# Kernel optimization log

Measured on AMD Instinct MI355X. Metric: run time of the kernel, lower is better.

Reference implementation:

```python
import jax, jax.numpy as jnp
import numpy as np

N = 100000
E = 1600000
IN_FEAT, HID, OUT = 256, 64, 32


def setup_inputs() -> dict:
    key = jax.random.key(0)
    k = jax.random.split(key, 6)
    x = jax.random.normal(k[0], (N, IN_FEAT), dtype=jnp.float32)
    edge_index = jax.random.randint(k[1], (2, E), 0, N, dtype=jnp.int64)
    # fc1: Linear(in_feat, hidden_feat)
    fc1_w = jax.random.normal(k[2], (HID, IN_FEAT), dtype=jnp.float32) / np.sqrt(IN_FEAT)
    fc1_b = jnp.zeros((HID,), dtype=jnp.float32)
    # GCNConv(hidden_feat, out_feat): weight [hid, out], bias [out]
    gcn_w = jax.random.normal(k[3], (HID, OUT), dtype=jnp.float32) / np.sqrt(HID)
    gcn_b = jnp.zeros((OUT,), dtype=jnp.float32)
    return {"x": x, "edge_index": edge_index, "fc1_w": fc1_w, "fc1_b": fc1_b,
            "gcn_w": gcn_w, "gcn_b": gcn_b}


def reference(x, edge_index, fc1_w, fc1_b, gcn_w, gcn_b):
    n = x.shape[0]
    # fc1: dense linear
    h = x @ fc1_w.T + fc1_b                      # [N, HID]
    # GCNConv linear transform
    hw = h @ gcn_w                               # [N, OUT]
    # add self-loops (PyG default add_self_loops=True)
    loop = jnp.arange(n, dtype=edge_index.dtype)
    src = jnp.concatenate([edge_index[0], loop])  # [E+N]
    dst = jnp.concatenate([edge_index[1], loop])
    # symmetric degree normalization: deg computed on dst (in-degree incl. self-loops)
    deg = jax.ops.segment_sum(jnp.ones_like(dst, dtype=hw.dtype), dst, num_segments=n)
    dinv = jnp.where(deg > 0, jax.lax.rsqrt(deg), 0.0)
    norm = dinv[src] * dinv[dst]                  # [E+N]
    # gather source features, scale, scatter-add to destinations
    msgs = hw[src] * norm[:, None]                # [E+N, OUT]
    out = jax.ops.segment_sum(msgs, dst, num_segments=n) + gcn_b
    return out
```

## Files before the change

kernel.cpp:

```cpp
#include <hip/hip_runtime.h>
#include <hip/hip_fp16.h>

constexpr int IN_FEAT = 256;
constexpr int HID     = 64;
constexpr int OUT     = 32;

typedef _Float16 half8 __attribute__((ext_vector_type(8)));
typedef float    f32x4 __attribute__((ext_vector_type(4)));

__global__ __launch_bounds__(256) void prep_W(
    const float* __restrict__ fc1_w,
    const float* __restrict__ fc1_b,
    const float* __restrict__ gcn_w,
    _Float16* __restrict__ wsw,
    float* __restrict__ bhw)
{
    int idx = blockIdx.x * 256 + threadIdx.x;
    int k = idx >> 5;
    int c = idx & 31;
    float acc = 0.f;
#pragma unroll
    for (int h = 0; h < HID; ++h)
        acc += fc1_w[h * IN_FEAT + k] * gcn_w[h * OUT + c];
    wsw[c * 256 + (((k >> 3) ^ (c & 7)) << 3) + (k & 7)] = (_Float16)acc;

    if (idx < OUT) {
        float b = 0.f;
#pragma unroll
        for (int h = 0; h < HID; ++h)
            b += fc1_b[h] * gcn_w[h * OUT + idx];
        bhw[idx] = b;
    }
}

__global__ __launch_bounds__(256) void zero_cnt(int* __restrict__ cnt, int n)
{
    int i = blockIdx.x * 256 + threadIdx.x;
    if (i < n) cnt[i] = 0;
}

__global__ __launch_bounds__(256) void count_deg(
    const int* __restrict__ dst, int* __restrict__ cnt, int E)
{
    int e = blockIdx.x * 256 + threadIdx.x;
    if (e < E) atomicAdd(&cnt[dst[e]], 1);
}

__global__ __launch_bounds__(256) void make_dinv(
    const int* __restrict__ cnt, float* __restrict__ dinv, int n)
{
    int i = blockIdx.x * 256 + threadIdx.x;
    if (i < n) dinv[i] = rsqrtf((float)(cnt[i] + 1));
}

__global__ __launch_bounds__(256) void gemm_mfma(
    const float* __restrict__ x,
    const _Float16* __restrict__ wsw,
    const float* __restrict__ bhw,
    const float* __restrict__ dinv,
    const float* __restrict__ gcn_b,
    _Float16* __restrict__ hw2,
    _Float16* __restrict__ oacc,
    int n)
{
    __shared__ __align__(16) _Float16 xs[64 * 256];
    __shared__ __align__(16) _Float16 wt[32 * 256];

    int t = threadIdx.x;

    {
        const float4* wg = reinterpret_cast<const float4*>(wsw);
        float4* wl = reinterpret_cast<float4*>(wt);
#pragma unroll
        for (int i = 0; i < 4; ++i)
            wl[t + 256 * i] = wg[t + 256 * i];
    }

    int row0 = blockIdx.x * 64;
    {
        int hwid = t >> 5;
        int lk   = t & 31;
        const float4* xg = reinterpret_cast<const float4*>(x);
        float4 A[8], B[8];
#pragma unroll
        for (int g = 0; g < 8; ++g) {
            int r = g * 8 + hwid;
            int row = row0 + r;
            A[g] = make_float4(0.f, 0.f, 0.f, 0.f);
            B[g] = make_float4(0.f, 0.f, 0.f, 0.f);
            if (row < n) {
                const float4* p = xg + (size_t)row * 64 + lk * 2;
                A[g] = p[0];
                B[g] = p[1];
            }
        }
        char* xsb = reinterpret_cast<char*>(xs);
#pragma unroll
        for (int g = 0; g < 8; ++g) {
            int r = g * 8 + hwid;
            half8 h;
            h[0] = (_Float16)A[g].x; h[1] = (_Float16)A[g].y;
            h[2] = (_Float16)A[g].z; h[3] = (_Float16)A[g].w;
            h[4] = (_Float16)B[g].x; h[5] = (_Float16)B[g].y;
            h[6] = (_Float16)B[g].z; h[7] = (_Float16)B[g].w;
            int slot = lk ^ (r & 7);
            *reinterpret_cast<half8*>(xsb + r * 512 + slot * 16) = h;
        }
    }
    __syncthreads();

    int l = t & 63;
    int w = t >> 6;
    int lr   = l & 15;
    int acol = l >> 4;
    int arow = (w << 4) | lr;
    int axor = arow & 7;
    int bxor = lr & 7;

    const char* xsb = reinterpret_cast<const char*>(xs);
    const char* wtb = reinterpret_cast<const char*>(wt);

    f32x4 acc0 = {0.f, 0.f, 0.f, 0.f};
    f32x4 acc1 = {0.f, 0.f, 0.f, 0.f};
#pragma unroll
    for (int ks = 0; ks < 8; ++ks) {
        int ak = (ks << 2) | acol;
        half8 Af = *reinterpret_cast<const half8*>(xsb + arow * 512 + ((ak ^ axor) << 4));
        half8 B0 = *reinterpret_cast<const half8*>(wtb + lr * 512 + ((ak ^ bxor) << 4));
        half8 B1 = *reinterpret_cast<const half8*>(wtb + (lr + 16) * 512 + ((ak ^ bxor) << 4));
        acc0 = __builtin_amdgcn_mfma_f32_16x16x32_f16(Af, B0, acc0, 0, 0, 0);
        acc1 = __builtin_amdgcn_mfma_f32_16x16x32_f16(Af, B1, acc1, 0, 0, 0);
    }

    int c0 = lr;
    int orow0 = row0 + (w << 4) + (acol << 2);
    float b0  = bhw[c0];
    float b1  = bhw[c0 + 16];
    float gb0 = gcn_b[c0];
    float gb1 = gcn_b[c0 + 16];
#pragma unroll
    for (int i = 0; i < 4; ++i) {
        int row = orow0 + i;
        if (row < n) {
            float h0 = acc0[i] + b0;
            float h1 = acc1[i] + b1;
            hw2[(size_t)row * OUT + c0]      = (_Float16)h0;
            hw2[(size_t)row * OUT + 16 + c0] = (_Float16)h1;
            float di = dinv[row];
            float d2 = di * di;
            oacc[(size_t)row * OUT + c0]      = (_Float16)(gb0 + d2 * h0);
            oacc[(size_t)row * OUT + 16 + c0] = (_Float16)(gb1 + d2 * h1);
        }
    }
}

__global__ __launch_bounds__(256) void scatter_f16(
    const int* __restrict__ src, const int* __restrict__ dst,
    const float* __restrict__ dinv,
    const __half2* __restrict__ hw2,
    __half2* __restrict__ oacc,
    int E)
{
    int t = blockIdx.x * 256 + threadIdx.x;
    int e = t >> 4;
    int c = t & 15;
    if (e >= E) return;
    int s = src[e];
    int d = dst[e];
    float w = dinv[s] * dinv[d];
    __half2 hv = hw2[(size_t)s * 16 + c];
    __half2 val = __floats2half2_rn(w * __low2float(hv), w * __high2float(hv));
    unsafeAtomicAdd(&oacc[(size_t)d * 16 + c], val);
}

__global__ __launch_bounds__(256) void convert_out(
    const __half2* __restrict__ oacc, float2* __restrict__ out, int n16)
{
    int i = blockIdx.x * 256 + threadIdx.x;
    if (i >= n16) return;
    __half2 h = oacc[i];
    out[i] = make_float2(__low2float(h), __high2float(h));
}

extern "C" void kernel_launch(void* const* d_in, const int* in_sizes, int n_in,
                              void* d_out, int out_size, void* d_ws, size_t ws_size,
                              hipStream_t stream)
{
    const float* x      = (const float*)d_in[0];
    const int*   eidx   = (const int*)d_in[1];
    const float* fc1_w  = (const float*)d_in[2];
    const float* fc1_b  = (const float*)d_in[3];
    const float* gcn_w  = (const float*)d_in[4];
    const float* gcn_b  = (const float*)d_in[5];
    float* out = (float*)d_out;

    int n = in_sizes[0] / IN_FEAT;
    int E = in_sizes[1] / 2;
    const int* src = eidx;
    const int* dst = eidx + E;

    auto align4 = [](size_t v) { return (v + 3) & ~(size_t)3; };
    float* ws = (float*)d_ws;
    size_t o = 0;
    _Float16* wsw  = (_Float16*)(ws + o); o = align4(o + 4096);
    float*    bhw  = ws + o;              o = align4(o + OUT);
    float*    dinv = ws + o;              o = align4(o + n);
    int*      cnt  = (int*)(ws + o);      o = align4(o + n);
    _Float16* hw2  = (_Float16*)(ws + o); o = align4(o + (size_t)n * OUT / 2);
    _Float16* oacc = (_Float16*)(ws + o); o = align4(o + (size_t)n * OUT / 2);
    (void)ws_size;

    dim3 blk(256);
    prep_W<<<dim3((IN_FEAT * OUT) / 256), blk, 0, stream>>>(fc1_w, fc1_b, gcn_w, wsw, bhw);
    zero_cnt<<<dim3((n + 255) / 256), blk, 0, stream>>>(cnt, n);
    count_deg<<<dim3((E + 255) / 256), blk, 0, stream>>>(dst, cnt, E);
    make_dinv<<<dim3((n + 255) / 256), blk, 0, stream>>>(cnt, dinv, n);
    gemm_mfma<<<dim3((n + 63) / 64), blk, 0, stream>>>(
        x, wsw, bhw, dinv, gcn_b, hw2, oacc, n);
    long long sthreads = (long long)E * 16;
    scatter_f16<<<dim3((int)((sthreads + 255) / 256)), blk, 0, stream>>>(
        src, dst, dinv, (const __half2*)hw2, (__half2*)oacc, E);
    int n16 = n * OUT / 2;
    convert_out<<<dim3((n16 + 255) / 256), blk, 0, stream>>>(
        (const __half2*)oacc, (float2*)out, n16);
}
```

Baseline: 337.8 us.

## Bin edges by destination bucket and accumulate scatter in shared memory

Replaces per-node global degree atomics and the global fp16 atomic scatter with a coarse counting sort of edges into 128-node destination buckets. Per-bucket kernels then compute degrees and accumulate messages in fp32 shared-memory slices, writing the final output directly. This also removes the separate convert kernel. Separately, the GEMM reads the weight matrix straight from global/L2 instead of staging it in LDS. The costs are an extra binning pass with global atomics, extra edge storage, a single-block scan, and load imbalance when buckets hold different edge counts.

```diff
diff --git a/kernel.cpp b/kernel.cpp
--- a/kernel.cpp
+++ b/kernel.cpp
@@ -4,6 +4,8 @@
 constexpr int IN_FEAT = 256;
 constexpr int HID     = 64;
 constexpr int OUT     = 32;
+constexpr int BSH     = 7;
+constexpr int BR      = 1 << BSH;
 
 typedef _Float16 half8 __attribute__((ext_vector_type(8)));
 typedef float    f32x4 __attribute__((ext_vector_type(4)));
@@ -12,7 +14,7 @@
     const float* __restrict__ fc1_w,
     const float* __restrict__ fc1_b,
     const float* __restrict__ gcn_w,
-    _Float16* __restrict__ wsw,
+    _Float16* __restrict__ wlin,
     float* __restrict__ bhw)
 {
     int idx = blockIdx.x * 256 + threadIdx.x;
@@ -22,7 +24,7 @@
 #pragma unroll
     for (int h = 0; h < HID; ++h)
         acc += fc1_w[h * IN_FEAT + k] * gcn_w[h * OUT + c];
-    wsw[c * 256 + (((k >> 3) ^ (c & 7)) << 3) + (k & 7)] = (_Float16)acc;
+    wlin[c * 256 + k] = (_Float16)acc;
 
     if (idx < OUT) {
         float b = 0.f;
@@ -33,29 +35,85 @@
     }
 }
 
-__global__ __launch_bounds__(256) void zero_cnt(int* __restrict__ cnt, int n)
+__global__ __launch_bounds__(256) void zero_i32(int* __restrict__ p, int n)
 {
     int i = blockIdx.x * 256 + threadIdx.x;
-    if (i < n) cnt[i] = 0;
-}
-
-__global__ __launch_bounds__(256) void count_deg(
-    const int* __restrict__ dst, int* __restrict__ cnt, int E)
+    if (i < n) p[i] = 0;
+}
+
+__global__ __launch_bounds__(256) void bucket_count(
+    const int* __restrict__ dst, int* __restrict__ bcnt, int E)
 {
     int e = blockIdx.x * 256 + threadIdx.x;
-    if (e < E) atomicAdd(&cnt[dst[e]], 1);
-}
-
-__global__ __launch_bounds__(256) void make_dinv(
-    const int* __restrict__ cnt, float* __restrict__ dinv, int n)
-{
-    int i = blockIdx.x * 256 + threadIdx.x;
-    if (i < n) dinv[i] = rsqrtf((float)(cnt[i] + 1));
+    if (e < E) atomicAdd(&bcnt[dst[e] >> BSH], 1);
+}
+
+__global__ __launch_bounds__(256) void bucket_scan(
+    const int* __restrict__ bcnt, int* __restrict__ off, int* __restrict__ cur,
+    int NB)
+{
+    int t = threadIdx.x;
+    int i = t * 4;
+    int c0 = (i     < NB) ? bcnt[i]     : 0;
+    int c1 = (i + 1 < NB) ? bcnt[i + 1] : 0;
+    int c2 = (i + 2 < NB) ? bcnt[i + 2] : 0;
+    int c3 = (i + 3 < NB) ? bcnt[i + 3] : 0;
+    int s = c0 + c1 + c2 + c3;
+    int lane = t & 63;
+    int incl = s;
+    for (int d = 1; d < 64; d <<= 1) {
+        int u = __shfl_up(incl, d, 64);
+        if (lane >= d) incl += u;
+    }
+    __shared__ int wtot[4];
+    if (lane == 63) wtot[t >> 6] = incl;
+    __syncthreads();
+    int w = t >> 6;
+    int wbase = 0;
+    for (int j = 0; j < 4; ++j) if (j < w) wbase += wtot[j];
+    int e0 = wbase + incl - s;
+
+    if (i     < NB) { off[i]     = e0;                cur[i]     = e0; }
+    if (i + 1 < NB) { off[i + 1] = e0 + c0;           cur[i + 1] = e0 + c0; }
+    if (i + 2 < NB) { off[i + 2] = e0 + c0 + c1;      cur[i + 2] = e0 + c0 + c1; }
+    if (i + 3 < NB) { off[i + 3] = e0 + c0 + c1 + c2; cur[i + 3] = e0 + c0 + c1 + c2; }
+    if (t == 0) off[NB] = wtot[0] + wtot[1] + wtot[2] + wtot[3];
+}
+
+__global__ __launch_bounds__(256) void bin_edges(
+    const int* __restrict__ src, const int* __restrict__ dst,
+    int* __restrict__ cur, int2* __restrict__ edata, int E)
+{
+    int e = blockIdx.x * 256 + threadIdx.x;
+    if (e >= E) return;
+    int s = src[e];
+    int d = dst[e];
+    int pos = atomicAdd(&cur[d >> BSH], 1);
+    edata[pos] = make_int2(s, d);
+}
+
+__global__ __launch_bounds__(256) void deg_dinv(
+    const int2* __restrict__ edata, const int* __restrict__ off,
+    float* __restrict__ dinv, int n)
+{
+    __shared__ int lcnt[BR];
+    int b = blockIdx.x;
+    int t = threadIdx.x;
+    if (t < BR) lcnt[t] = 0;
+    __syncthreads();
+    int beg = off[b], end = off[b + 1];
+    for (int e = beg + t; e < end; e += 256)
+        atomicAdd(&lcnt[edata[e].y & (BR - 1)], 1);
+    __syncthreads();
+    if (t < BR) {
+        int node = (b << BSH) + t;
+        if (node < n) dinv[node] = rsqrtf((float)(lcnt[t] + 1));
+    }
 }
 
 __global__ __launch_bounds__(256) void gemm_mfma(
     const float* __restrict__ x,
-    const _Float16* __restrict__ wsw,
+    const _Float16* __restrict__ wlin,
     const float* __restrict__ bhw,
     const float* __restrict__ dinv,
     const float* __restrict__ gcn_b,
@@ -64,19 +122,10 @@
     int n)
 {
     __shared__ __align__(16) _Float16 xs[64 * 256];
-    __shared__ __align__(16) _Float16 wt[32 * 256];
-
-    int t = threadIdx.x;
-
-    {
-        const float4* wg = reinterpret_cast<const float4*>(wsw);
-        float4* wl = reinterpret_cast<float4*>(wt);
-#pragma unroll
-        for (int i = 0; i < 4; ++i)
-            wl[t + 256 * i] = wg[t + 256 * i];
-    }
-
+
+    int t = threadIdx.x;
     int row0 = blockIdx.x * 64;
+
     {
         int hwid = t >> 5;
         int lk   = t & 31;
@@ -115,10 +164,10 @@
     int acol = l >> 4;
     int arow = (w << 4) | lr;
     int axor = arow & 7;
-    int bxor = lr & 7;
 
     const char* xsb = reinterpret_cast<const char*>(xs);
-    const char* wtb = reinterpret_cast<const char*>(wt);
+    const _Float16* wb0 = wlin + lr * 256;
+    const _Float16* wb1 = wlin + (lr + 16) * 256;
 
     f32x4 acc0 = {0.f, 0.f, 0.f, 0.f};
     f32x4 acc1 = {0.f, 0.f, 0.f, 0.f};
@@ -126,8 +175,8 @@
     for (int ks = 0; ks < 8; ++ks) {
         int ak = (ks << 2) | acol;
         half8 Af = *reinterpret_cast<const half8*>(xsb + arow * 512 + ((ak ^ axor) << 4));
-        half8 B0 = *reinterpret_cast<const half8*>(wtb + lr * 512 + ((ak ^ bxor) << 4));
-        half8 B1 = *reinterpret_cast<const half8*>(wtb + (lr + 16) * 512 + ((ak ^ bxor) << 4));
+        half8 B0 = *reinterpret_cast<const half8*>(wb0 + (ak << 3));
+        half8 B1 = *reinterpret_cast<const half8*>(wb1 + (ak << 3));
         acc0 = __builtin_amdgcn_mfma_f32_16x16x32_f16(Af, B0, acc0, 0, 0, 0);
         acc1 = __builtin_amdgcn_mfma_f32_16x16x32_f16(Af, B1, acc1, 0, 0, 0);
     }
@@ -154,32 +203,50 @@
     }
 }
 
-__global__ __launch_bounds__(256) void scatter_f16(
-    const int* __restrict__ src, const int* __restrict__ dst,
-    const float* __restrict__ dinv,
-    const __half2* __restrict__ hw2,
-    __half2* __restrict__ oacc,
-    int E)
-{
-    int t = blockIdx.x * 256 + threadIdx.x;
-    int e = t >> 4;
-    int c = t & 15;
-    if (e >= E) return;
-    int s = src[e];
-    int d = dst[e];
-    float w = dinv[s] * dinv[d];
-    __half2 hv = hw2[(size_t)s * 16 + c];
-    __half2 val = __floats2half2_rn(w * __low2float(hv), w * __high2float(hv));
-    unsafeAtomicAdd(&oacc[(size_t)d * 16 + c], val);
-}
-
-__global__ __launch_bounds__(256) void convert_out(
-    const __half2* __restrict__ oacc, float2* __restrict__ out, int n16)
-{
-    int i = blockIdx.x * 256 + threadIdx.x;
-    if (i >= n16) return;
-    __half2 h = oacc[i];
-    out[i] = make_float2(__low2float(h), __high2float(h));
+__global__ __launch_bounds__(256) void scatter_bucket(
+    const int2* __restrict__ edata, const int* __restrict__ off,
+    const float* __restrict__ dinv, const _Float16* __restrict__ hw2,
+    const _Float16* __restrict__ oacc, float* __restrict__ out, int n)
+{
+    __shared__ float slice[BR * OUT];
+
+    int b = blockIdx.x;
+    int t = threadIdx.x;
+    for (int i = t; i < BR * OUT; i += 256) slice[i] = 0.f;
+    __syncthreads();
+
+    int beg = off[b], end = off[b + 1];
+    int g = t >> 5;
+    int c = t & 31;
+
+    auto process = [&](int e) {
+        int2 rec = edata[e];
+        int s = rec.x;
+        int d = rec.y;
+        float wgt = dinv[s] * dinv[d];
+        float hv = (float)hw2[(size_t)s * OUT + c];
+        atomicAdd(&slice[((d & (BR - 1)) << 5) + c], wgt * hv);
+    };
+
+    int e = beg + g;
+    for (; e + 24 < end; e += 32) {
+        process(e);
+        process(e + 8);
+        process(e + 16);
+        process(e + 24);
+    }
+    for (; e < end; e += 8) process(e);
+    __syncthreads();
+
+    int base = b << BSH;
+#pragma unroll
+    for (int j = 0; j < BR * OUT / 256; ++j) {
+        int idx = j * 256 + t;
+        int node = base + (idx >> 5);
+        int cc = idx & 31;
+        if (node < n)
+            out[(size_t)node * OUT + cc] = (float)oacc[(size_t)node * OUT + cc] + slice[idx];
+    }
 }
 
 extern "C" void kernel_launch(void* const* d_in, const int* in_sizes, int n_in,
@@ -198,29 +265,31 @@
     int E = in_sizes[1] / 2;
     const int* src = eidx;
     const int* dst = eidx + E;
+    int NB = (n + BR - 1) >> BSH;
 
     auto align4 = [](size_t v) { return (v + 3) & ~(size_t)3; };
     float* ws = (float*)d_ws;
     size_t o = 0;
-    _Float16* wsw  = (_Float16*)(ws + o); o = align4(o + 4096);
+    _Float16* wlin = (_Float16*)(ws + o); o = align4(o + 4096);
     float*    bhw  = ws + o;              o = align4(o + OUT);
     float*    dinv = ws + o;              o = align4(o + n);
-    int*      cnt  = (int*)(ws + o);      o = align4(o + n);
+    int*      bcnt = (int*)(ws + o);      o = align4(o + NB);
+    int*      off  = (int*)(ws + o);      o = align4(o + NB + 1);
+    int*      cur  = (int*)(ws + o);      o = align4(o + NB);
+    int2*     edata = (int2*)(ws + o);    o = align4(o + (size_t)2 * E);
     _Float16* hw2  = (_Float16*)(ws + o); o = align4(o + (size_t)n * OUT / 2);
     _Float16* oacc = (_Float16*)(ws + o); o = align4(o + (size_t)n * OUT / 2);
     (void)ws_size;
 
     dim3 blk(256);
-    prep_W<<<dim3((IN_FEAT * OUT) / 256), blk, 0, stream>>>(fc1_w, fc1_b, gcn_w, wsw, bhw);
-    zero_cnt<<<dim3((n + 255) / 256), blk, 0, stream>>>(cnt, n);
-    count_deg<<<dim3((E + 255) / 256), blk, 0, stream>>>(dst, cnt, E);
-    make_dinv<<<dim3((n + 255) / 256), blk, 0, stream>>>(cnt, dinv, n);
+    prep_W<<<dim3((IN_FEAT * OUT) / 256), blk, 0, stream>>>(fc1_w, fc1_b, gcn_w, wlin, bhw);
+    zero_i32<<<dim3((NB + 255) / 256), blk, 0, stream>>>(bcnt, NB);
+    bucket_count<<<dim3((E + 255) / 256), blk, 0, stream>>>(dst, bcnt, E);
+    bucket_scan<<<dim3(1), blk, 0, stream>>>(bcnt, off, cur, NB);
+    bin_edges<<<dim3((E + 255) / 256), blk, 0, stream>>>(src, dst, cur, edata, E);
+    deg_dinv<<<dim3(NB), blk, 0, stream>>>(edata, off, dinv, n);
     gemm_mfma<<<dim3((n + 63) / 64), blk, 0, stream>>>(
-        x, wsw, bhw, dinv, gcn_b, hw2, oacc, n);
-    long long sthreads = (long long)E * 16;
-    scatter_f16<<<dim3((int)((sthreads + 255) / 256)), blk, 0, stream>>>(
-        src, dst, dinv, (const __half2*)hw2, (__half2*)oacc, E);
-    int n16 = n * OUT / 2;
-    convert_out<<<dim3((n16 + 255) / 256), blk, 0, stream>>>(
-        (const __half2*)oacc, (float2*)out, n16);
-}
+        x, wlin, bhw, dinv, gcn_b, hw2, oacc, n);
+    scatter_bucket<<<dim3(NB), blk, 0, stream>>>(
+        edata, off, dinv, hw2, oacc, out, n);
+}
```

Result: slower. 1.293 ms (+282.7%).
